# Optimization experiments

Hardware: AMD Instinct MI355X
Metric: run time of the kernel (lower is better)

## Reference

```python
import jax, jax.numpy as jnp
import numpy as np

D_MODEL = 1024
NUM_HEADS = 16
D_K = D_MODEL // NUM_HEADS


def setup_inputs() -> dict:
    key = jax.random.key(0)
    ks = jax.random.split(key, 11)
    B, T = 4, 2048
    s = 1.0 / np.sqrt(D_MODEL)
    inp = {
        "query": jax.random.normal(ks[0], (B, T, D_MODEL), jnp.float32),
        "key": jax.random.normal(ks[1], (B, T, D_MODEL), jnp.float32),
        "value": jax.random.normal(ks[2], (B, T, D_MODEL), jnp.float32),
        "Wq": jax.random.uniform(ks[3], (D_MODEL, D_MODEL), jnp.float32, -s, s),
        "bq": jax.random.uniform(ks[4], (D_MODEL,), jnp.float32, -s, s),
        "Wk": jax.random.uniform(ks[5], (D_MODEL, D_MODEL), jnp.float32, -s, s),
        "bk": jax.random.uniform(ks[6], (D_MODEL,), jnp.float32, -s, s),
        "Wv": jax.random.uniform(ks[7], (D_MODEL, D_MODEL), jnp.float32, -s, s),
        "bv": jax.random.uniform(ks[8], (D_MODEL,), jnp.float32, -s, s),
        "Wo": jax.random.uniform(ks[9], (D_MODEL, D_MODEL), jnp.float32, -s, s),
        "bo": jax.random.uniform(ks[10], (D_MODEL,), jnp.float32, -s, s),
    }
    return inp


def _split_heads(x):
    B, T, _ = x.shape
    return x.reshape(B, T, NUM_HEADS, D_K).transpose(0, 2, 1, 3)  # (B,H,T,dk)


def reference(query, key, value, Wq, bq, Wk, bk, Wv, bv, Wo, bo):
    q = _split_heads(query @ Wq + bq)   # (B,H,Tq,dk)
    k = _split_heads(key @ Wk + bk)     # (B,H,Tk,dk)
    v = _split_heads(value @ Wv + bv)   # (B,H,Tk,dk)
    scale = 1.0 / jnp.sqrt(jnp.asarray(D_K, q.dtype))
    scores = jnp.einsum("bhqd,bhkd->bhqk", q, k) * scale
    weights = jax.nn.softmax(scores, axis=-1)
    attn = jnp.einsum("bhqk,bhkd->bhqd", weights, v)  # (B,H,Tq,dk)
    B, H, T, dk = attn.shape
    attn = attn.transpose(0, 2, 1, 3).reshape(B, T, H * dk)
    return attn @ Wo + bo
```

## Files before the change

kernel.cpp:

```cpp
#include <hip/hip_runtime.h>
#include <hip/hip_bf16.h>
#include <stdint.h>


typedef __bf16 bf16x8 __attribute__((ext_vector_type(8)));
typedef short  v4s    __attribute__((ext_vector_type(4)));
typedef float  f32x4  __attribute__((ext_vector_type(4)));

#define LOG2E 1.44269504088896340736f

static __device__ __forceinline__ uint32_t f2bf(float x) {
  uint32_t u = __float_as_uint(x);
  u += 0x7fffu + ((u >> 16) & 1u);
  return u >> 16;
}
#if __has_builtin(__builtin_amdgcn_cvt_pk_bf16_f32)
static __device__ __forceinline__ uint32_t pk2bf(float a, float b) {
  typedef __bf16 b2 __attribute__((ext_vector_type(2)));
  union { b2 v; uint32_t u; } x;
  x.v = __builtin_amdgcn_cvt_pk_bf16_f32(a, b);
  return x.u;
}
#else
static __device__ __forceinline__ uint32_t pk2bf(float a, float b) {
  return f2bf(a) | (f2bf(b) << 16);
}
#endif
static __device__ __forceinline__ void gl2lds16(const void* g, void* l) {
  __builtin_amdgcn_global_load_lds(
      (const __attribute__((address_space(1))) uint32_t*)g,
      (__attribute__((address_space(3))) uint32_t*)l, 16, 0, 0);
}

__global__ void convert_inputs(const float* __restrict__ q, const float* __restrict__ k,
                               const float* __restrict__ v, uint16_t* __restrict__ qo,
                               uint16_t* __restrict__ ko, uint16_t* __restrict__ vo) {
  const float* src = blockIdx.y == 0 ? q : (blockIdx.y == 1 ? k : v);
  uint16_t*    dst = blockIdx.y == 0 ? qo : (blockIdx.y == 1 ? ko : vo);
  size_t idx = ((size_t)blockIdx.x * 256 + threadIdx.x) * 8;
  float4 a = *(const float4*)(src + idx);
  float4 b = *(const float4*)(src + idx + 4);
  uint4 o;
  o.x = pk2bf(a.x, a.y); o.y = pk2bf(a.z, a.w);
  o.z = pk2bf(b.x, b.y); o.w = pk2bf(b.z, b.w);
  *(uint4*)(dst + idx) = o;
}

__global__ void transpose_weights(const float* __restrict__ Wq, const float* __restrict__ Wk,
                                  const float* __restrict__ Wv, const float* __restrict__ Wo,
                                  uint16_t* __restrict__ out) {
  __shared__ float t[32][33];
  const float* W = blockIdx.z == 0 ? Wq : blockIdx.z == 1 ? Wk : blockIdx.z == 2 ? Wv : Wo;
  uint16_t* O = out + (size_t)blockIdx.z * 1048576;
  int tx = threadIdx.x & 31, ty = threadIdx.x >> 5;
  int r0 = blockIdx.y * 32, c0 = blockIdx.x * 32;
#pragma unroll
  for (int i = 0; i < 4; i++) t[ty + i * 8][tx] = W[(size_t)(r0 + ty + i * 8) * 1024 + c0 + tx];
  __syncthreads();
#pragma unroll
  for (int i = 0; i < 4; i++)
    O[(size_t)(c0 + ty + i * 8) * 1024 + r0 + tx] = (uint16_t)f2bf(t[tx][ty + i * 8]);
}

static __device__ __forceinline__ void gemm_body(
    const uint16_t* __restrict__ A, const uint16_t* __restrict__ Bt,
    const float* __restrict__ bias, void* __restrict__ Cout,
    int N, int K, int mode, float oscale, int mBase, int nBase,
    uint16_t* __restrict__ lA, uint16_t* __restrict__ lB) {
  int tid = threadIdx.x, wave = tid >> 6, lane = tid & 63;
  int q = lane >> 4, c = lane & 15;
  int wrow = wave & 1, wcol = wave >> 1;
  f32x4 acc[4][4] = {};

  int swz = ((lane & 7) ^ (lane >> 3)) * 8;
  const uint16_t* gA = A + (size_t)(mBase + wave * 32 + (lane >> 3)) * K + swz;
  const uint16_t* gB = Bt + (size_t)(nBase + wave * 32 + (lane >> 3)) * K + swz;
  int cs = c & 7;

  for (int kt = 0; kt < K / 64; kt++) {
    __syncthreads();
    int k0 = kt * 64;
#pragma unroll
    for (int it = 0; it < 4; it++) {
      gl2lds16(gA + (size_t)(it * 8) * K + k0, &lA[(wave * 32 + it * 8) * 64]);
      gl2lds16(gB + (size_t)(it * 8) * K + k0, &lB[(wave * 32 + it * 8) * 64]);
    }
    __syncthreads();
#pragma unroll
    for (int kk = 0; kk < 2; kk++) {
      bf16x8 af[4], bfr[4];
#pragma unroll
      for (int i = 0; i < 4; i++)
        af[i] = *(const bf16x8*)&lA[(wrow * 64 + i * 16 + c) * 64 + ((kk * 4 + q) ^ cs) * 8];
#pragma unroll
      for (int j = 0; j < 4; j++)
        bfr[j] = *(const bf16x8*)&lB[(wcol * 64 + j * 16 + c) * 64 + ((kk * 4 + q) ^ cs) * 8];
#pragma unroll
      for (int i = 0; i < 4; i++)
#pragma unroll
        for (int j = 0; j < 4; j++)
          acc[i][j] = __builtin_amdgcn_mfma_f32_16x16x32_bf16(af[i], bfr[j], acc[i][j], 0, 0, 0);
    }
  }

  float bb[4];
#pragma unroll
  for (int j = 0; j < 4; j++) bb[j] = bias[nBase + wcol * 64 + j * 16 + c];

  if (mode == 0) {
    float* Co = (float*)Cout;
#pragma unroll
    for (int i = 0; i < 4; i++)
#pragma unroll
      for (int j = 0; j < 4; j++) {
        int row = mBase + wrow * 64 + i * 16 + q * 4;
        int col = nBase + wcol * 64 + j * 16 + c;
#pragma unroll
        for (int r = 0; r < 4; r++) Co[(size_t)(row + r) * N + col] = acc[i][j][r] + bb[j];
      }
  } else if (mode == 1) {
    uint16_t* Co = (uint16_t*)Cout;
#pragma unroll
    for (int i = 0; i < 4; i++)
#pragma unroll
      for (int j = 0; j < 4; j++) {
        int row = mBase + wrow * 64 + i * 16 + q * 4;
        int col = nBase + wcol * 64 + j * 16 + c;
#pragma unroll
        for (int r = 0; r < 4; r++)
          Co[(size_t)(row + r) * N + col] = (uint16_t)f2bf((acc[i][j][r] + bb[j]) * oscale);
      }
  } else {
    uint16_t* Co = (uint16_t*)Cout;
#pragma unroll
    for (int i = 0; i < 4; i++)
#pragma unroll
      for (int j = 0; j < 4; j++) {
        int n = nBase + wcol * 64 + j * 16 + c;
        int h = n >> 6, d = n & 63;
        int m = mBase + wrow * 64 + i * 16 + q * 4;
        int b = m >> 11, t = m & 2047;
        uint32_t lo = pk2bf(acc[i][j][0] + bb[j], acc[i][j][1] + bb[j]);
        uint32_t hi = pk2bf(acc[i][j][2] + bb[j], acc[i][j][3] + bb[j]);
        *(uint2*)(Co + (size_t)((b * 16 + h) * 64 + d) * 2048 + t) = make_uint2(lo, hi);
      }
  }
}

__global__ __launch_bounds__(256, 2)
void gemm_qkv(const uint16_t* __restrict__ qb, const uint16_t* __restrict__ kb,
              const uint16_t* __restrict__ vb, const uint16_t* __restrict__ Wtq,
              const uint16_t* __restrict__ Wtk, const uint16_t* __restrict__ Wtv,
              const float* __restrict__ bq, const float* __restrict__ bk,
              const float* __restrict__ bv, uint16_t* __restrict__ Qp,
              uint16_t* __restrict__ Kp, uint16_t* __restrict__ Vt, float cs) {
  __shared__ uint16_t lA[8192], lB[8192];
  int z = blockIdx.z;
  const uint16_t* A  = z == 0 ? qb : (z == 1 ? kb : vb);
  const uint16_t* Bt = z == 0 ? Wtq : (z == 1 ? Wtk : Wtv);
  const float* bias  = z == 0 ? bq : (z == 1 ? bk : bv);
  void* C            = z == 0 ? (void*)Qp : (z == 1 ? (void*)Kp : (void*)Vt);
  int mode   = z == 2 ? 2 : 1;
  float os   = z == 0 ? cs : 1.0f;
  gemm_body(A, Bt, bias, C, 1024, 1024, mode, os, blockIdx.y * 128, blockIdx.x * 128, lA, lB);
}

__global__ __launch_bounds__(256, 2)
void gemm_out(const uint16_t* __restrict__ A, const uint16_t* __restrict__ Bt,
              const float* __restrict__ bias, float* __restrict__ C) {
  __shared__ uint16_t lA[8192], lB[8192];
  gemm_body(A, Bt, bias, C, 1024, 1024, 0, 1.0f, blockIdx.y * 128, blockIdx.x * 128, lA, lB);
}

__global__ __launch_bounds__(256, 2)
void attn(const uint16_t* __restrict__ Qp, const uint16_t* __restrict__ Kp,
          const uint16_t* __restrict__ Vt, uint16_t* __restrict__ Ob) {
  __shared__ uint16_t sK[128 * 64], sV[64 * 128];
  int tid = threadIdx.x, wave = tid >> 6, lane = tid & 63;
  int q = lane >> 4, c = lane & 15;
  int cs = c & 7;
  int bh = blockIdx.y, b = bh >> 4, h = bh & 15;
  int qbase = blockIdx.x * 128;
  int swz = ((lane & 7) ^ (lane >> 3)) * 8;

  {
    const uint16_t* gQ =
        Qp + (size_t)(b * 2048 + qbase + wave * 32 + (lane >> 3)) * 1024 + h * 64 + swz;
#pragma unroll
    for (int it = 0; it < 4; it++)
      gl2lds16(gQ + (size_t)(it * 8) * 1024, &sK[(wave * 32 + it * 8) * 64]);
  }
  __syncthreads();
  bf16x8 qf[2][2];
#pragma unroll
  for (int it = 0; it < 2; it++)
#pragma unroll
    for (int kk = 0; kk < 2; kk++)
      qf[it][kk] =
          *(const bf16x8*)&sK[(wave * 32 + it * 16 + c) * 64 + ((kk * 4 + q) ^ cs) * 8];

  f32x4 o[4][2] = {};
  float rs0 = 0.f, rs1 = 0.f;

  const uint16_t* gK0 =
      Kp + (size_t)(b * 2048 + wave * 32 + (lane >> 3)) * 1024 + h * 64 + swz;
  const uint16_t* gV0 = Vt + (size_t)(bh * 64 + wave * 16 + q) * 2048;

  for (int kt = 0; kt < 16; kt++) {
    __syncthreads();
#pragma unroll
    for (int it = 0; it < 4; it++)
      gl2lds16(gK0 + (size_t)(kt * 128 + it * 8) * 1024, &sK[(wave * 32 + it * 8) * 64]);
#pragma unroll
    for (int it = 0; it < 4; it++) {
      int vch = (c ^ (((it & 1) * 4) | q)) * 8;
      gl2lds16(gV0 + (size_t)(it * 4) * 2048 + kt * 128 + vch,
               &sV[(wave * 16 + it * 4) * 128]);
    }
    __syncthreads();

#pragma unroll
    for (int jt = 0; jt < 8; jt++) {
      bf16x8 a0 = *(const bf16x8*)&sK[(jt * 16 + c) * 64 + (q ^ cs) * 8];
      bf16x8 a1 = *(const bf16x8*)&sK[(jt * 16 + c) * 64 + ((4 + q) ^ cs) * 8];
      f32x4 s0 = __builtin_amdgcn_mfma_f32_16x16x32_bf16(a0, qf[0][0],
                                                         (f32x4){0.f, 0.f, 0.f, 0.f}, 0, 0, 0);
      s0 = __builtin_amdgcn_mfma_f32_16x16x32_bf16(a1, qf[0][1], s0, 0, 0, 0);
      f32x4 s1 = __builtin_amdgcn_mfma_f32_16x16x32_bf16(a0, qf[1][0],
                                                         (f32x4){0.f, 0.f, 0.f, 0.f}, 0, 0, 0);
      s1 = __builtin_amdgcn_mfma_f32_16x16x32_bf16(a1, qf[1][1], s1, 0, 0, 0);

      float p00 = __builtin_amdgcn_exp2f(s0[0]), p01 = __builtin_amdgcn_exp2f(s0[1]);
      float p02 = __builtin_amdgcn_exp2f(s0[2]), p03 = __builtin_amdgcn_exp2f(s0[3]);
      float p10 = __builtin_amdgcn_exp2f(s1[0]), p11 = __builtin_amdgcn_exp2f(s1[1]);
      float p12 = __builtin_amdgcn_exp2f(s1[2]), p13 = __builtin_amdgcn_exp2f(s1[3]);
      rs0 += (p00 + p01) + (p02 + p03);
      rs1 += (p10 + p11) + (p12 + p13);
      union { uint32_t u[2]; v4s s4; } pb0, pb1;
      pb0.u[0] = pk2bf(p00, p01); pb0.u[1] = pk2bf(p02, p03);
      pb1.u[0] = pk2bf(p10, p11); pb1.u[1] = pk2bf(p12, p13);

#pragma unroll
      for (int mt = 0; mt < 4; mt++) {
        v4s a = *(const v4s*)&sV[(mt * 16 + c) * 128 + (((jt * 2 + (q >> 1)) ^ cs) * 8) +
                                 (q & 1) * 4];
        o[mt][0] = __builtin_amdgcn_mfma_f32_16x16x16bf16_1k(a, pb0.s4, o[mt][0], 0, 0, 0);
        o[mt][1] = __builtin_amdgcn_mfma_f32_16x16x16bf16_1k(a, pb1.s4, o[mt][1], 0, 0, 0);
      }
    }
  }

  rs0 += __shfl_xor(rs0, 16); rs0 += __shfl_xor(rs0, 32);
  rs1 += __shfl_xor(rs1, 16); rs1 += __shfl_xor(rs1, 32);
  float l[2] = {rs0, rs1};

#pragma unroll
  for (int it = 0; it < 2; it++) {
    float inv = 1.0f / l[it];
    size_t trow = (size_t)(b * 2048 + qbase + wave * 32 + it * 16 + c) * 1024 + h * 64;
#pragma unroll
    for (int mt = 0; mt < 4; mt++) {
      uint32_t lo = pk2bf(o[mt][it][0] * inv, o[mt][it][1] * inv);
      uint32_t hi = pk2bf(o[mt][it][2] * inv, o[mt][it][3] * inv);
      *(uint2*)(Ob + trow + mt * 16 + q * 4) = make_uint2(lo, hi);
    }
  }
}

extern "C" void kernel_launch(void* const* d_in, const int* in_sizes, int n_in,
                              void* d_out, int out_size, void* d_ws, size_t ws_size,
                              hipStream_t stream) {
  (void)in_sizes; (void)n_in; (void)out_size; (void)ws_size;
  const float* query = (const float*)d_in[0];
  const float* key_  = (const float*)d_in[1];
  const float* value = (const float*)d_in[2];
  const float* Wq = (const float*)d_in[3]; const float* bq = (const float*)d_in[4];
  const float* Wk = (const float*)d_in[5]; const float* bk = (const float*)d_in[6];
  const float* Wv = (const float*)d_in[7]; const float* bv = (const float*)d_in[8];
  const float* Wo = (const float*)d_in[9]; const float* bo = (const float*)d_in[10];

  const size_t SZ = (size_t)8192 * 1024;
  uint16_t* buf0 = (uint16_t*)d_ws;
  uint16_t* buf1 = buf0 + SZ;
  uint16_t* buf2 = buf1 + SZ;
  uint16_t* buf3 = buf2 + SZ;
  uint16_t* wts  = buf3 + SZ;
  uint16_t* Wtq = wts;
  uint16_t* Wtk = wts + 1048576;
  uint16_t* Wtv = wts + 2097152;
  uint16_t* Wto = wts + 3145728;
  uint16_t* Kp  = wts + 4194304;
  uint16_t* Vt  = Kp + SZ;

  const float Cs = 0.125f * LOG2E;

  convert_inputs<<<dim3(4096, 3), 256, 0, stream>>>(query, key_, value, buf0, buf1, buf2);
  transpose_weights<<<dim3(32, 32, 4), 256, 0, stream>>>(Wq, Wk, Wv, Wo, wts);
  gemm_qkv<<<dim3(8, 64, 3), 256, 0, stream>>>(buf0, buf1, buf2, Wtq, Wtk, Wtv,
                                               bq, bk, bv, buf3, Kp, Vt, Cs);
  attn<<<dim3(16, 64), 256, 0, stream>>>(buf3, Kp, Vt, buf2);
  gemm_out<<<dim3(8, 64), 256, 0, stream>>>(buf2, Wto, bo, (float*)d_out);
}
```

Measured before the change: 360.6 us.

## Double-buffer K/V tiles in attention and remap blocks for L2 locality

The attention kernel now streams K and V in 64-key tiles through a double-buffered shared-memory region. The next tile's global-to-LDS copy is issued before computing on the current one, so each iteration needs one barrier instead of two and load latency overlaps with MFMA work. Block IDs are also remapped so that neighbouring blocks in launch order are spread across (batch, head, q-tile) in a strided pattern, aiming at better L2 reuse of K/V. In exchange there are twice as many loop iterations with smaller tiles, and the single barrier must correctly cover buffer reuse.

Result: no change. 355.1 us (-1.5%).

```diff
diff --git a/kernel.cpp b/kernel.cpp
--- a/kernel.cpp
+++ b/kernel.cpp
@@ -175,12 +175,16 @@
 __global__ __launch_bounds__(256, 2)
 void attn(const uint16_t* __restrict__ Qp, const uint16_t* __restrict__ Kp,
           const uint16_t* __restrict__ Vt, uint16_t* __restrict__ Ob) {
-  __shared__ uint16_t sK[128 * 64], sV[64 * 128];
+  __shared__ uint16_t lds[16384];
   int tid = threadIdx.x, wave = tid >> 6, lane = tid & 63;
   int q = lane >> 4, c = lane & 15;
   int cs = c & 7;
-  int bh = blockIdx.y, b = bh >> 4, h = bh & 15;
-  int qbase = blockIdx.x * 128;
+
+  int id = blockIdx.y * 16 + blockIdx.x;
+  int wk = (id & 7) * 128 + (id >> 3);
+  int qt = wk & 15, bh = wk >> 4;
+  int b = bh >> 4, h = bh & 15;
+  int qbase = qt * 128;
   int swz = ((lane & 7) ^ (lane >> 3)) * 8;
 
   {
@@ -188,7 +192,7 @@
         Qp + (size_t)(b * 2048 + qbase + wave * 32 + (lane >> 3)) * 1024 + h * 64 + swz;
 #pragma unroll
     for (int it = 0; it < 4; it++)
-      gl2lds16(gQ + (size_t)(it * 8) * 1024, &sK[(wave * 32 + it * 8) * 64]);
+      gl2lds16(gQ + (size_t)(it * 8) * 1024, &lds[(wave * 32 + it * 8) * 64]);
   }
   __syncthreads();
   bf16x8 qf[2][2];
@@ -197,32 +201,44 @@
 #pragma unroll
     for (int kk = 0; kk < 2; kk++)
       qf[it][kk] =
-          *(const bf16x8*)&sK[(wave * 32 + it * 16 + c) * 64 + ((kk * 4 + q) ^ cs) * 8];
+          *(const bf16x8*)&lds[(wave * 32 + it * 16 + c) * 64 + ((kk * 4 + q) ^ cs) * 8];
+  __syncthreads();
 
   f32x4 o[4][2] = {};
   float rs0 = 0.f, rs1 = 0.f;
 
   const uint16_t* gK0 =
-      Kp + (size_t)(b * 2048 + wave * 32 + (lane >> 3)) * 1024 + h * 64 + swz;
-  const uint16_t* gV0 = Vt + (size_t)(bh * 64 + wave * 16 + q) * 2048;
-
-  for (int kt = 0; kt < 16; kt++) {
+      Kp + (size_t)(b * 2048 + wave * 16 + (lane >> 3)) * 1024 + h * 64 + swz;
+  const uint16_t* gV0 = Vt + (size_t)(bh * 64 + wave * 16 + (lane >> 3)) * 2048 + swz;
+
+#pragma unroll
+  for (int it = 0; it < 2; it++) {
+    gl2lds16(gK0 + (size_t)(it * 8) * 1024, &lds[(wave * 16 + it * 8) * 64]);
+    gl2lds16(gV0 + (size_t)(it * 8) * 2048, &lds[8192 + (wave * 16 + it * 8) * 64]);
+  }
+
+  for (int kt = 0; kt < 32; kt++) {
+    int cur = kt & 1;
     __syncthreads();
-#pragma unroll
-    for (int it = 0; it < 4; it++)
-      gl2lds16(gK0 + (size_t)(kt * 128 + it * 8) * 1024, &sK[(wave * 32 + it * 8) * 64]);
-#pragma unroll
-    for (int it = 0; it < 4; it++) {
-      int vch = (c ^ (((it & 1) * 4) | q)) * 8;
-      gl2lds16(gV0 + (size_t)(it * 4) * 2048 + kt * 128 + vch,
-               &sV[(wave * 16 + it * 4) * 128]);
-    }
-    __syncthreads();
-
-#pragma unroll
-    for (int jt = 0; jt < 8; jt++) {
-      bf16x8 a0 = *(const bf16x8*)&sK[(jt * 16 + c) * 64 + (q ^ cs) * 8];
-      bf16x8 a1 = *(const bf16x8*)&sK[(jt * 16 + c) * 64 + ((4 + q) ^ cs) * 8];
+
+    if (kt < 31) {
+      int nb = (cur ^ 1) * 4096;
+#pragma unroll
+      for (int it = 0; it < 2; it++) {
+        gl2lds16(gK0 + (size_t)((kt + 1) * 64 + it * 8) * 1024,
+                 &lds[nb + (wave * 16 + it * 8) * 64]);
+        gl2lds16(gV0 + (size_t)(it * 8) * 2048 + (kt + 1) * 64,
+                 &lds[8192 + nb + (wave * 16 + it * 8) * 64]);
+      }
+    }
+
+    const uint16_t* sKc = &lds[cur * 4096];
+    const uint16_t* sVc = &lds[8192 + cur * 4096];
+
+#pragma unroll
+    for (int jt = 0; jt < 4; jt++) {
+      bf16x8 a0 = *(const bf16x8*)&sKc[(jt * 16 + c) * 64 + (q ^ cs) * 8];
+      bf16x8 a1 = *(const bf16x8*)&sKc[(jt * 16 + c) * 64 + ((4 + q) ^ cs) * 8];
       f32x4 s0 = __builtin_amdgcn_mfma_f32_16x16x32_bf16(a0, qf[0][0],
                                                          (f32x4){0.f, 0.f, 0.f, 0.f}, 0, 0, 0);
       s0 = __builtin_amdgcn_mfma_f32_16x16x32_bf16(a1, qf[0][1], s0, 0, 0, 0);
@@ -242,8 +258,8 @@
 
 #pragma unroll
       for (int mt = 0; mt < 4; mt++) {
-        v4s a = *(const v4s*)&sV[(mt * 16 + c) * 128 + (((jt * 2 + (q >> 1)) ^ cs) * 8) +
-                                 (q & 1) * 4];
+        v4s a = *(const v4s*)&sVc[(mt * 16 + c) * 64 + (((jt * 2 + (q >> 1)) ^ cs) * 8) +
+                                  (q & 1) * 4];
         o[mt][0] = __builtin_amdgcn_mfma_f32_16x16x16bf16_1k(a, pb0.s4, o[mt][0], 0, 0, 0);
         o[mt][1] = __builtin_amdgcn_mfma_f32_16x16x16bf16_1k(a, pb1.s4, o[mt][1], 0, 0, 0);
       }
```
